# Kernel optimization log

Measured on AMD Instinct MI355X. Metric: run time of the kernel, lower is better.

## Reference

```python
import jax, jax.numpy as jnp
import numpy as np

N_NODES = 10000
N_EDGES = 320000
D_IN = 256
D_HID = 256
N_CLASSES = 40


def _init_linear(key, fan_in, fan_out):
    kw, kb = jax.random.split(key)
    bound = 1.0 / np.sqrt(fan_in)
    W = jax.random.uniform(kw, (fan_in, fan_out), jnp.float32, -bound, bound)
    b = jax.random.uniform(kb, (fan_out,), jnp.float32, -bound, bound)
    return W, b


def setup_inputs() -> dict:
    key = jax.random.key(0)
    k0, k1, k2, k3, k4 = jax.random.split(key, 5)
    node_features = jax.random.normal(k0, (N_NODES, D_IN), jnp.float32)
    edge_index = jax.random.randint(k1, (2, N_EDGES), 0, N_NODES, jnp.int64)
    W1, b1 = _init_linear(k2, D_IN, D_HID)
    W2, b2 = _init_linear(k3, D_HID, D_HID)
    W3, b3 = _init_linear(k4, D_HID, N_CLASSES)
    return {"node_features": node_features, "edge_index": edge_index,
            "W1": W1, "b1": b1, "W2": W2, "b2": b2, "W3": W3, "b3": b3}


def _mp_layer(x, src, dst, W, b):
    # message: linear transform of source-node features (transform-then-gather
    # is mathematically identical to gather-then-transform and cheaper when E>N)
    msg = (x @ W + b)[src]                      # [E, d_out]
    # scatter sum-aggregate messages at destination nodes
    out = jax.ops.segment_sum(msg, dst, num_segments=N_NODES)  # [N, d_out]
    return out


def reference(node_features, edge_index, W1, b1, W2, b2, W3, b3):
    src, dst = edge_index[0], edge_index[1]
    x = jax.nn.relu(_mp_layer(node_features, src, dst, W1, b1))
    x = jax.nn.relu(_mp_layer(x, src, dst, W2, b2))
    x = jax.nn.relu(_mp_layer(x, src, dst, W3, b3))
    return x
```

## Files before the change

### kernel.cpp

```cpp
#include <hip/hip_runtime.h>


#define N_NODES   10000
#define N_EDGES   320000
#define D_HID     256
#define N_CLASSES 40
#define CAP       96
#define DUMMY     10000

typedef __attribute__((ext_vector_type(8))) short short8;
typedef __attribute__((ext_vector_type(4))) float f32x4;

__device__ __forceinline__ ushort f2bf(float f) {
    unsigned u = __float_as_uint(f);
    u = (u + 0x7fffu + ((u >> 16) & 1u)) >> 16;
    return (ushort)u;
}
__device__ __forceinline__ float bf2f(ushort u) {
    return __uint_as_float(((unsigned)u) << 16);
}


__global__ __launch_bounds__(256)
void prep_kernel(const float* __restrict__ X,
                 const float* __restrict__ W1, const float* __restrict__ W2,
                 const float* __restrict__ W3,
                 ushort* __restrict__ Xb, ushort* __restrict__ bufY,
                 ushort* __restrict__ bufH,
                 ushort* __restrict__ W1b, ushort* __restrict__ W2b,
                 ushort* __restrict__ W3b, int* __restrict__ cursor) {
    const int tid  = blockIdx.x * 256 + threadIdx.x;
    const int nthr = gridDim.x * 256;
    for (int i = tid; i < N_NODES; i += nthr) cursor[i] = 0;
    ushort4 z; z.x = 0; z.y = 0; z.z = 0; z.w = 0;
    if (tid < 64) {
        ((ushort4*)Xb)[640000 + tid]   = z;
        ((ushort4*)bufY)[640000 + tid] = z;
    }
    if (tid < 10) ((ushort4*)bufH)[100000 + tid] = z;
    for (int i = tid; i < N_NODES * D_HID / 4; i += nthr) {
        float4 v = ((const float4*)X)[i];
        ushort4 o;
        o.x = f2bf(v.x); o.y = f2bf(v.y); o.z = f2bf(v.z); o.w = f2bf(v.w);
        ((ushort4*)Xb)[i] = o;
    }
    for (int i = tid; i < 141312; i += nthr) {
        if (i < 65536) {
            int n = i >> 8, k = i & 255;
            W1b[i] = f2bf(W1[k * 256 + n]);
        } else if (i < 131072) {
            int t2 = i - 65536;
            int n = t2 >> 8, k = t2 & 255;
            W2b[t2] = f2bf(W2[k * 256 + n]);
        } else {
            int t2 = i - 131072;
            int n = t2 >> 8, k = t2 & 255;
            W3b[t2] = f2bf(W3[k * N_CLASSES + n]);
        }
    }
}


__global__ __launch_bounds__(256)
void place_kernel(const int* __restrict__ edges, int* __restrict__ cursor,
                  int* __restrict__ esrc) {
    int e = blockIdx.x * 256 + threadIdx.x;
    if (e < N_EDGES) {
        int d = edges[N_EDGES + e];
        int pos = atomicAdd(&cursor[d], 1);
        if (pos < CAP) esrc[d * CAP + pos] = edges[e];
    }
}


__global__ __launch_bounds__(256)
void gather_kernel(const ushort* __restrict__ Xin, const int* __restrict__ deg,
                   const int* __restrict__ esrc, ushort* __restrict__ Ag,
                   float* __restrict__ degOut) {
    __shared__ int eidx[4 * CAP];
    __shared__ int degL[4];

    const int tid  = threadIdx.x;
    const int w    = tid >> 6, lane = tid & 63;
    const int lo   = lane & 31, hi = lane >> 5;
    const int base = blockIdx.x * 4;
    const uint4* hp4 = (const uint4*)Xin;

    {
        int i = blockIdx.x * 256 + tid;
        if (i < 320000) {
            uint4 t = hp4[i];
            asm volatile("" :: "v"(t.x), "v"(t.y), "v"(t.z), "v"(t.w));
        }
    }

    for (int i = tid; i < 4 * CAP; i += 256)
        eidx[i] = esrc[base * CAP + i];
    if (tid < 4) degL[tid] = deg[base + tid];
    __syncthreads();

    const int node = base + w;
    const int raw  = degL[w];
    const int cnt  = raw < CAP ? raw : CAP;
    const int nb   = (cnt + 15) >> 4;

    float a[8] = {};
    for (int b = 0; b < nb; ++b) {
        uint4 v[8];
#pragma unroll
        for (int u = 0; u < 8; ++u) {
            int slot = b * 16 + 2 * u + hi;
            int e = (slot < cnt) ? eidx[w * CAP + slot] : DUMMY;
            v[u] = hp4[(size_t)e * 32 + lo];
        }
#pragma unroll
        for (int u = 0; u < 8; ++u) {
            a[0] += bf2f((ushort)(v[u].x & 0xffff)); a[1] += bf2f((ushort)(v[u].x >> 16));
            a[2] += bf2f((ushort)(v[u].y & 0xffff)); a[3] += bf2f((ushort)(v[u].y >> 16));
            a[4] += bf2f((ushort)(v[u].z & 0xffff)); a[5] += bf2f((ushort)(v[u].z >> 16));
            a[6] += bf2f((ushort)(v[u].w & 0xffff)); a[7] += bf2f((ushort)(v[u].w >> 16));
        }
    }
#pragma unroll
    for (int j = 0; j < 8; ++j) a[j] += __shfl_xor(a[j], 32);
    if (lane < 32) {
        uint4 o;
        o.x = (unsigned)f2bf(a[0]) | ((unsigned)f2bf(a[1]) << 16);
        o.y = (unsigned)f2bf(a[2]) | ((unsigned)f2bf(a[3]) << 16);
        o.z = (unsigned)f2bf(a[4]) | ((unsigned)f2bf(a[5]) << 16);
        o.w = (unsigned)f2bf(a[6]) | ((unsigned)f2bf(a[7]) << 16);
        ((uint4*)(Ag + (size_t)node * 256))[lo] = o;
    }
    if (lane == 0) degOut[node] = (float)raw;
}


#define LDSB 264

template<bool CHAIN>
__global__ __launch_bounds__(512)
void gemm_kernel(const ushort* __restrict__ Ag, const ushort* __restrict__ Bt,
                 const float* __restrict__ bias, const float* __restrict__ degF,
                 const ushort* __restrict__ W3b, const float* __restrict__ b3,
                 ushort* __restrict__ Out) {
    __shared__ ushort Bs[256 * LDSB];
    __shared__ ushort W3L[40 * LDSB];
    __shared__ float  degL[64];

    const int tid  = threadIdx.x;
    const int wave = tid >> 6, lane = tid & 63;
    const int lr = lane & 15, lg = lane >> 4;
    const int rg = wave >> 1, cg = wave & 1;
    const int rowBase = blockIdx.x * 64;

#pragma unroll
    for (int p = 0; p < 16; ++p) {
        int idx = p * 512 + tid;
        int n = idx >> 5, c = (idx & 31) * 8;
        *(uint4*)(Bs + n * LDSB + c) = *(const uint4*)(Bt + (size_t)n * 256 + c);
    }
    if (CHAIN) {
#pragma unroll
        for (int p = 0; p < 3; ++p) {
            int idx = p * 512 + tid;
            if (idx < 1280) {
                int n = idx >> 5, c = (idx & 31) * 8;
                *(uint4*)(W3L + n * LDSB + c) = *(const uint4*)(W3b + (size_t)n * 256 + c);
            }
        }
    }
    if (tid < 64) degL[tid] = degF[rowBase + tid];

    short8 afr[8];
    const size_t aBase = (size_t)(rowBase + rg * 16 + lr) * 256 + lg * 8;
#pragma unroll
    for (int ks = 0; ks < 8; ++ks)
        afr[ks] = *(const short8*)(Ag + aBase + ks * 32);

    __syncthreads();

    f32x4 acc[8] = {};
#pragma unroll
    for (int ks = 0; ks < 8; ++ks) {
        int k0 = ks * 32;
#pragma unroll
        for (int j = 0; j < 8; ++j) {
            short8 bf = *(const short8*)(Bs + (cg * 128 + j * 16 + lr) * LDSB + k0 + lg * 8);
            acc[j] = __builtin_amdgcn_mfma_f32_16x16x32_bf16(afr[ks], bf, acc[j], 0, 0, 0);
        }
    }

    if (!CHAIN) {
#pragma unroll
        for (int j = 0; j < 8; ++j) {
            int col = cg * 128 + j * 16 + lr;
            float bv = bias[col];
#pragma unroll
            for (int r = 0; r < 4; ++r) {
                int rl = rg * 16 + lg * 4 + r;
                int grow = rowBase + rl;
                if (grow < N_NODES)
                    Out[(size_t)grow * 256 + col] =
                        f2bf(fmaxf(fmaf(degL[rl], bv, acc[j][r]), 0.f));
            }
        }
    } else {
        __syncthreads();
#pragma unroll
        for (int j = 0; j < 8; ++j) {
            int col = cg * 128 + j * 16 + lr;
            float bv = bias[col];
#pragma unroll
            for (int r = 0; r < 4; ++r) {
                int rl = rg * 16 + lg * 4 + r;
                Bs[rl * LDSB + col] = f2bf(fmaxf(fmaf(degL[rl], bv, acc[j][r]), 0.f));
            }
        }
        __syncthreads();
        for (int t = wave; t < 12; t += 8) {
            int rT = t & 3, cT = t >> 2;
            f32x4 a3 = {};
#pragma unroll
            for (int ks = 0; ks < 8; ++ks) {
                short8 af = *(const short8*)(Bs + (rT * 16 + lr) * LDSB + ks * 32 + lg * 8);
                short8 bf = *(const short8*)(W3L + (cT * 16 + lr) * LDSB + ks * 32 + lg * 8);
                a3 = __builtin_amdgcn_mfma_f32_16x16x32_bf16(af, bf, a3, 0, 0, 0);
            }
            int col = cT * 16 + lr;
            if (col < N_CLASSES) {
                float bv = b3[col];
#pragma unroll
                for (int r = 0; r < 4; ++r) {
                    int grow = rowBase + rT * 16 + lg * 4 + r;
                    if (grow < N_NODES)
                        Out[(size_t)grow * N_CLASSES + col] = f2bf(a3[r] + bv);
                }
            }
        }
    }
}


__global__ __launch_bounds__(256)
void agg_relu_40_kernel(const ushort* __restrict__ h, const int* __restrict__ deg,
                        const int* __restrict__ esrc, float* __restrict__ out) {
    const int wv   = threadIdx.x >> 6;
    const int lane = threadIdx.x & 63;
    const int node = (blockIdx.x << 2) + wv;
    const int l6   = (lane < 60) ? lane : 0;
    const int g6   = l6 / 10;
    const int c10  = l6 - g6 * 10;

    int cnt = deg[node];
    if (cnt > CAP) cnt = CAP;
    const int* ep = esrc + node * CAP;
    float a0 = 0.f, a1 = 0.f, a2 = 0.f, a3 = 0.f;
    for (int b = 0; b < cnt; b += 6) {
        int slot = b + g6;
        int s = (slot < cnt) ? ep[slot] : DUMMY;
        uint2 v = *(const uint2*)(h + (size_t)s * N_CLASSES + c10 * 4);
        a0 += bf2f((ushort)(v.x & 0xffff)); a1 += bf2f((ushort)(v.x >> 16));
        a2 += bf2f((ushort)(v.y & 0xffff)); a3 += bf2f((ushort)(v.y >> 16));
    }
#define FOLD40(x) { x += __shfl(x, lane + 30);                      \
                    float t1 = __shfl(x, lane + 10);                \
                    float t2 = __shfl(x, lane + 20);                \
                    x += t1 + t2; }
    FOLD40(a0); FOLD40(a1); FOLD40(a2); FOLD40(a3);
#undef FOLD40
    if (lane < 10) {
        float4 o;
        o.x = fmaxf(a0, 0.f); o.y = fmaxf(a1, 0.f);
        o.z = fmaxf(a2, 0.f); o.w = fmaxf(a3, 0.f);
        *(float4*)(out + (size_t)node * N_CLASSES + lane * 4) = o;
    }
}


extern "C" void kernel_launch(void* const* d_in, const int* in_sizes, int n_in,
                              void* d_out, int out_size, void* d_ws, size_t ws_size,
                              hipStream_t stream) {
    const float* X     = (const float*)d_in[0];
    const int*   edges = (const int*)d_in[1];
    const float* W1 = (const float*)d_in[2];
    const float* b1 = (const float*)d_in[3];
    const float* W2 = (const float*)d_in[4];
    const float* b2 = (const float*)d_in[5];
    const float* W3 = (const float*)d_in[6];
    const float* b3 = (const float*)d_in[7];
    float* out = (float*)d_out;

    char* ws = (char*)d_ws;
    ushort* Xb    = (ushort*)(ws);
    ushort* bufY  = (ushort*)(ws + 5120512);
    ushort* bufH  = (ushort*)(ws + 10241024);
    ushort* W1b   = (ushort*)(ws + 11041104);
    ushort* W2b   = (ushort*)(ws + 11172176);
    ushort* W3b   = (ushort*)(ws + 11303248);
    int*    cursor= (int*)(ws + 11323728);
    int*    esrc  = (int*)(ws + 11363728);
    ushort* Ag1   = (ushort*)(ws + 15203728);
    ushort* Ag2   = (ushort*)(ws + 20348304);
    float*  degF  = (float*)(ws + 25492880);

    prep_kernel<<<512, 256, 0, stream>>>(X, W1, W2, W3, Xb, bufY, bufH,
                                         W1b, W2b, W3b, cursor);
    place_kernel<<<(N_EDGES + 255) / 256, 256, 0, stream>>>(edges, cursor, esrc);
    gather_kernel<<<N_NODES / 4, 256, 0, stream>>>(Xb, cursor, esrc, Ag1, degF);
    gemm_kernel<false><<<157, 512, 0, stream>>>(Ag1, W1b, b1, degF, W3b, b3, bufY);
    gather_kernel<<<N_NODES / 4, 256, 0, stream>>>(bufY, cursor, esrc, Ag2, degF);
    gemm_kernel<true><<<157, 512, 0, stream>>>(Ag2, W2b, b2, degF, W3b, b3, bufH);
    agg_relu_40_kernel<<<N_NODES / 4, 256, 0, stream>>>(bufH, cursor, esrc, out);
}
```

Measured before the change: 159.2 us.

## Split neighbor gather into two column-half passes with nontemporal index traffic

The feature-gather kernel is split into two launches, each aggregating one 128-column half of the 256-wide bf16 rows. Each half-row is fetched by 16 lanes, with four edges per wave in flight. The aim is to halve the working set touched per pass so gathered rows stay cache-resident. The edge-index writes, the index loads and the aggregate stores now use nontemporal hints, and the explicit L2 prefetch of the input is removed. This costs an extra launch per layer, rereads the edge lists twice, and adds a two-step shuffle reduction.

```diff
diff --git a/kernel.cpp b/kernel.cpp
--- a/kernel.cpp
+++ b/kernel.cpp
@@ -10,6 +10,7 @@
 
 typedef __attribute__((ext_vector_type(8))) short short8;
 typedef __attribute__((ext_vector_type(4))) float f32x4;
+typedef __attribute__((ext_vector_type(4))) unsigned u32x4;
 
 __device__ __forceinline__ ushort f2bf(float f) {
     unsigned u = __float_as_uint(f);
@@ -68,34 +69,26 @@
     if (e < N_EDGES) {
         int d = edges[N_EDGES + e];
         int pos = atomicAdd(&cursor[d], 1);
-        if (pos < CAP) esrc[d * CAP + pos] = edges[e];
+        if (pos < CAP) __builtin_nontemporal_store(edges[e], &esrc[d * CAP + pos]);
     }
 }
 
 
 __global__ __launch_bounds__(256)
-void gather_kernel(const ushort* __restrict__ Xin, const int* __restrict__ deg,
-                   const int* __restrict__ esrc, ushort* __restrict__ Ag,
-                   float* __restrict__ degOut) {
+void gather_half_kernel(const ushort* __restrict__ Xin, const int* __restrict__ deg,
+                        const int* __restrict__ esrc, ushort* __restrict__ Ag,
+                        float* __restrict__ degOut, int colOff) {
     __shared__ int eidx[4 * CAP];
     __shared__ int degL[4];
 
     const int tid  = threadIdx.x;
     const int w    = tid >> 6, lane = tid & 63;
-    const int lo   = lane & 31, hi = lane >> 5;
+    const int eg   = lane >> 4;
+    const int cg   = lane & 15;
     const int base = blockIdx.x * 4;
-    const uint4* hp4 = (const uint4*)Xin;
-
-    {
-        int i = blockIdx.x * 256 + tid;
-        if (i < 320000) {
-            uint4 t = hp4[i];
-            asm volatile("" :: "v"(t.x), "v"(t.y), "v"(t.z), "v"(t.w));
-        }
-    }
 
     for (int i = tid; i < 4 * CAP; i += 256)
-        eidx[i] = esrc[base * CAP + i];
+        eidx[i] = __builtin_nontemporal_load(&esrc[base * CAP + i]);
     if (tid < 4) degL[tid] = deg[base + tid];
     __syncthreads();
 
@@ -103,18 +96,19 @@
     const int raw  = degL[w];
     const int cnt  = raw < CAP ? raw : CAP;
     const int nb   = (cnt + 15) >> 4;
+    const uint4* hp4 = (const uint4*)(Xin + colOff);
 
     float a[8] = {};
     for (int b = 0; b < nb; ++b) {
-        uint4 v[8];
-#pragma unroll
-        for (int u = 0; u < 8; ++u) {
-            int slot = b * 16 + 2 * u + hi;
+        uint4 v[4];
+#pragma unroll
+        for (int u = 0; u < 4; ++u) {
+            int slot = b * 16 + u * 4 + eg;
             int e = (slot < cnt) ? eidx[w * CAP + slot] : DUMMY;
-            v[u] = hp4[(size_t)e * 32 + lo];
-        }
-#pragma unroll
-        for (int u = 0; u < 8; ++u) {
+            v[u] = hp4[(size_t)e * 32 + cg];
+        }
+#pragma unroll
+        for (int u = 0; u < 4; ++u) {
             a[0] += bf2f((ushort)(v[u].x & 0xffff)); a[1] += bf2f((ushort)(v[u].x >> 16));
             a[2] += bf2f((ushort)(v[u].y & 0xffff)); a[3] += bf2f((ushort)(v[u].y >> 16));
             a[4] += bf2f((ushort)(v[u].z & 0xffff)); a[5] += bf2f((ushort)(v[u].z >> 16));
@@ -122,16 +116,19 @@
         }
     }
 #pragma unroll
-    for (int j = 0; j < 8; ++j) a[j] += __shfl_xor(a[j], 32);
-    if (lane < 32) {
-        uint4 o;
+    for (int j = 0; j < 8; ++j) {
+        a[j] += __shfl_xor(a[j], 16);
+        a[j] += __shfl_xor(a[j], 32);
+    }
+    if (lane < 16) {
+        u32x4 o;
         o.x = (unsigned)f2bf(a[0]) | ((unsigned)f2bf(a[1]) << 16);
         o.y = (unsigned)f2bf(a[2]) | ((unsigned)f2bf(a[3]) << 16);
         o.z = (unsigned)f2bf(a[4]) | ((unsigned)f2bf(a[5]) << 16);
         o.w = (unsigned)f2bf(a[6]) | ((unsigned)f2bf(a[7]) << 16);
-        ((uint4*)(Ag + (size_t)node * 256))[lo] = o;
-    }
-    if (lane == 0) degOut[node] = (float)raw;
+        __builtin_nontemporal_store(o, (u32x4*)(Ag + (size_t)node * 256 + colOff) + cg);
+    }
+    if (colOff == 0 && lane == 0) degOut[node] = (float)raw;
 }
 
 
@@ -306,9 +303,11 @@
     prep_kernel<<<512, 256, 0, stream>>>(X, W1, W2, W3, Xb, bufY, bufH,
                                          W1b, W2b, W3b, cursor);
     place_kernel<<<(N_EDGES + 255) / 256, 256, 0, stream>>>(edges, cursor, esrc);
-    gather_kernel<<<N_NODES / 4, 256, 0, stream>>>(Xb, cursor, esrc, Ag1, degF);
+    gather_half_kernel<<<N_NODES / 4, 256, 0, stream>>>(Xb, cursor, esrc, Ag1, degF, 0);
+    gather_half_kernel<<<N_NODES / 4, 256, 0, stream>>>(Xb, cursor, esrc, Ag1, degF, 128);
     gemm_kernel<false><<<157, 512, 0, stream>>>(Ag1, W1b, b1, degF, W3b, b3, bufY);
-    gather_kernel<<<N_NODES / 4, 256, 0, stream>>>(bufY, cursor, esrc, Ag2, degF);
+    gather_half_kernel<<<N_NODES / 4, 256, 0, stream>>>(bufY, cursor, esrc, Ag2, degF, 0);
+    gather_half_kernel<<<N_NODES / 4, 256, 0, stream>>>(bufY, cursor, esrc, Ag2, degF, 128);
     gemm_kernel<true><<<157, 512, 0, stream>>>(Ag2, W2b, b2, degF, W3b, b3, bufH);
     agg_relu_40_kernel<<<N_NODES / 4, 256, 0, stream>>>(bufH, cursor, esrc, out);
 }
```

Measured after the change: 173.7 us. 9.1% more time.
